# Kernel optimization log

Hardware: AMD Instinct MI355X
Metric: run time of the kernel (lower is better)

## Reference

```python
import jax, jax.numpy as jnp
import numpy as np

DIM = 1024
NUM_HEADS = 16
DPH = DIM // NUM_HEADS
B, S = 4, 2048
LN_EPS = 1e-5


def layer_norm(x, g, b):
    mu = jnp.mean(x, axis=-1, keepdims=True)
    var = jnp.mean((x - mu) ** 2, axis=-1, keepdims=True)
    return (x - mu) * jax.lax.rsqrt(var + LN_EPS) * g + b


def setup_inputs() -> dict:
    key = jax.random.key(0)
    ks = jax.random.split(key, 10)
    sd = 0.02
    return {
        "x": jax.random.normal(ks[0], (B, S, DIM), dtype=jnp.float32),
        "Wq": jax.random.normal(ks[1], (DIM, DIM), dtype=jnp.float32) * sd,
        "Wk": jax.random.normal(ks[2], (DIM, DIM), dtype=jnp.float32) * sd,
        "Wv": jax.random.normal(ks[3], (DIM, DIM), dtype=jnp.float32) * sd,
        "bq": jnp.zeros((DIM,), dtype=jnp.float32),
        "bk": jnp.zeros((DIM,), dtype=jnp.float32),
        "bv": jnp.zeros((DIM,), dtype=jnp.float32),
        "ln1_g": jnp.ones((DIM,), dtype=jnp.float32),
        "ln1_b": jnp.zeros((DIM,), dtype=jnp.float32),
        "W1": jax.random.normal(ks[4], (DIM, 4 * DIM), dtype=jnp.float32) * sd,
        "b1": jnp.zeros((4 * DIM,), dtype=jnp.float32),
        "W2": jax.random.normal(ks[5], (4 * DIM, DIM), dtype=jnp.float32) * sd,
        "b2": jnp.zeros((DIM,), dtype=jnp.float32),
        "ln2_g": jnp.ones((DIM,), dtype=jnp.float32),
        "ln2_b": jnp.zeros((DIM,), dtype=jnp.float32),
    }


def reference(x, Wq, Wk, Wv, bq, bk, bv, ln1_g, ln1_b, W1, b1, W2, b2, ln2_g, ln2_b):
    b, s, d = x.shape
    # QKV projections (heads are independent linears -> one fused GEMM each)
    q = (x @ Wq + bq).reshape(b, s, NUM_HEADS, DPH)
    k = (x @ Wk + bk).reshape(b, s, NUM_HEADS, DPH)
    v = (x @ Wv + bv).reshape(b, s, NUM_HEADS, DPH)
    # Faithful quirk: module scales by 1/sqrt(dph) twice => 1/dph total
    scores = jnp.einsum("bqhd,bkhd->bhqk", q, k) / DPH
    causal = jnp.tril(jnp.ones((s, s), dtype=bool))
    scores = jnp.where(causal, scores, -1e9)
    attn = jax.nn.softmax(scores, axis=-1)
    out_attn = jnp.einsum("bhqk,bkhd->bqhd", attn, v).reshape(b, s, d)
    # Add & Norm 1 (no output projection in original)
    h = layer_norm(out_attn + x, ln1_g, ln1_b)
    # Feed-forward (dropout is identity at eval)
    ffn = jax.nn.relu(h @ W1 + b1) @ W2 + b2
    # Add & Norm 2
    return layer_norm(ffn + h, ln2_g, ln2_b)
```

## Files before the change

### kernel.cpp

```cpp
#include <hip/hip_runtime.h>
#include <hip/hip_bf16.h>

typedef __bf16 bf16_t;
typedef __bf16 bf16x8 __attribute__((ext_vector_type(8)));
typedef __bf16 bf16x4 __attribute__((ext_vector_type(4)));
typedef float  floatx4 __attribute__((ext_vector_type(4)));

#define DIM    1024
#define S_LEN  2048
#define NHEAD  16

template <typename T>
__device__ __forceinline__ bf16x8 load8bf(const T* src) {
  if constexpr (sizeof(T) == 2) {
    return *reinterpret_cast<const bf16x8*>(src);
  } else {
    floatx4 f0 = *reinterpret_cast<const floatx4*>(src);
    floatx4 f1 = *reinterpret_cast<const floatx4*>(src + 4);
    bf16x8 h;
    h[0] = (bf16_t)f0[0]; h[1] = (bf16_t)f0[1];
    h[2] = (bf16_t)f0[2]; h[3] = (bf16_t)f0[3];
    h[4] = (bf16_t)f1[0]; h[5] = (bf16_t)f1[1];
    h[6] = (bf16_t)f1[2]; h[7] = (bf16_t)f1[3];
    return h;
  }
}

__device__ __forceinline__ void gll16(const bf16_t* g, bf16_t* l) {
  __builtin_amdgcn_global_load_lds(
      (const __attribute__((address_space(1))) void*)g,
      (__attribute__((address_space(3))) void*)l, 16, 0, 0);
}

__global__ __launch_bounds__(256) void conv_bf(const float* __restrict__ in,
                                               bf16_t* __restrict__ out) {
  size_t i = ((size_t)blockIdx.x * 256 + threadIdx.x) * 8;
  *reinterpret_cast<bf16x8*>(out + i) = load8bf(in + i);
}

__global__ __launch_bounds__(256) void convT3(
    const float* __restrict__ in0, int ldi0, bf16_t* __restrict__ out0,
    const float* __restrict__ in1, int ldi1, bf16_t* __restrict__ out1,
    const float* __restrict__ in2, int ldi2, bf16_t* __restrict__ out2,
    int ldo) {
  __shared__ bf16_t tile[32][33];
  const int z = blockIdx.z;
  const float* in = (z == 0) ? in0 : ((z == 1) ? in1 : in2);
  bf16_t* out = (z == 0) ? out0 : ((z == 1) ? out1 : out2);
  int ldi = (z == 0) ? ldi0 : ((z == 1) ? ldi1 : ldi2);
  int tx = threadIdx.x, ty = threadIdx.y;
  int n0 = blockIdx.x * 32, k0 = blockIdx.y * 32;
#pragma unroll
  for (int i = 0; i < 4; ++i)
    tile[ty + 8 * i][tx] = (bf16_t)in[(size_t)(k0 + ty + 8 * i) * ldi + n0 + tx];
  __syncthreads();
#pragma unroll
  for (int i = 0; i < 4; ++i)
    out[(size_t)(n0 + ty + 8 * i) * ldo + k0 + tx] = tile[tx][ty + 8 * i];
}

#define BM 128
#define BN 128
#define BK 32
#define LSTR 40

template <typename TA>
__global__ __launch_bounds__(256) void gemm_abt(
    const TA* __restrict__ A, int lda,
    const bf16_t* __restrict__ Bt, int zBRow,
    bf16_t* __restrict__ C, int ldc, int zCOff,
    const float* __restrict__ bias0, const float* __restrict__ bias1,
    const float* __restrict__ bias2,
    int K, int relu, int accum) {
  constexpr int ASTR = (sizeof(TA) == 2) ? BK : LSTR;
  __shared__ bf16_t As[BM * LSTR];
  __shared__ bf16_t Bs[BN * BK];
  const int z = blockIdx.z;
  const float* bias = (z == 0) ? bias0 : ((z == 1) ? bias1 : bias2);
  const bf16_t* Bz = Bt + (size_t)z * zBRow * K;
  C += (size_t)z * zCOff;

  const int tid  = threadIdx.x;
  const int lane = tid & 63;
  const int wave = tid >> 6;
  const int wr   = wave >> 1;
  const int wc   = wave & 1;
  const int quad = lane >> 4;
  const int l15  = lane & 15;
  const int m0   = blockIdx.y * BM;
  const int n0   = blockIdx.x * BN;

  floatx4 acc[4][4];
#pragma unroll
  for (int i = 0; i < 4; ++i)
#pragma unroll
    for (int j = 0; j < 4; ++j) acc[i][j] = (floatx4)(0.0f);

  const int kIters = K / BK;
  for (int kt = 0; kt < kIters; ++kt) {
#pragma unroll
    for (int i = 0; i < 2; ++i)
      gll16(Bz + (size_t)(n0 + wave * 32 + i * 16 + (lane >> 2)) * K +
                kt * BK + (lane & 3) * 8,
            &Bs[(wave * 32 + i * 16) * BK]);
    if constexpr (sizeof(TA) == 2) {
#pragma unroll
      for (int i = 0; i < 2; ++i)
        gll16(A + (size_t)(m0 + wave * 32 + i * 16 + (lane >> 2)) * lda +
                  kt * BK + (lane & 3) * 8,
              &As[(wave * 32 + i * 16) * BK]);
    } else {
#pragma unroll
      for (int p = 0; p < 2; ++p) {
        int id  = p * 256 + tid;
        int row = id >> 2;
        int c8  = (id & 3) * 8;
        *reinterpret_cast<bf16x8*>(&As[row * LSTR + c8]) =
            load8bf(A + (size_t)(m0 + row) * lda + kt * BK + c8);
      }
    }
    __syncthreads();

    bf16x8 a[4], b[4];
#pragma unroll
    for (int i = 0; i < 4; ++i)
      a[i] = *reinterpret_cast<const bf16x8*>(
          &As[(wr * 64 + i * 16 + l15) * ASTR + quad * 8]);
#pragma unroll
    for (int j = 0; j < 4; ++j)
      b[j] = *reinterpret_cast<const bf16x8*>(
          &Bs[(wc * 64 + j * 16 + l15) * BK + quad * 8]);
#pragma unroll
    for (int i = 0; i < 4; ++i)
#pragma unroll
      for (int j = 0; j < 4; ++j)
        acc[i][j] = __builtin_amdgcn_mfma_f32_16x16x32_bf16(a[i], b[j], acc[i][j], 0, 0, 0);
    __syncthreads();
  }

#pragma unroll
  for (int j = 0; j < 4; ++j) {
    int gn = n0 + wc * 64 + j * 16 + l15;
    float bv = bias ? bias[gn] : 0.0f;
#pragma unroll
    for (int i = 0; i < 4; ++i) {
      int gm = m0 + wr * 64 + i * 16 + quad * 4;
#pragma unroll
      for (int r = 0; r < 4; ++r) {
        float v = acc[i][j][r] + bv;
        if (relu) v = fmaxf(v, 0.0f);
        size_t idx = (size_t)(gm + r) * ldc + gn;
        if (accum) v += (float)C[idx];
        C[idx] = (bf16_t)v;
      }
    }
  }
}

__global__ __launch_bounds__(256) void transpose_v(const bf16_t* __restrict__ in,
                                                   bf16_t* __restrict__ outp) {
  __shared__ bf16_t tile[32][33];
  int tx = threadIdx.x, ty = threadIdx.y;
  int s0 = blockIdx.x * 32, d0 = blockIdx.y * 32, bh = blockIdx.z;
  int z = bh >> 4, h = bh & 15;
  const bf16_t* src = in + (size_t)z * S_LEN * 3072 + 2048 + h * 64;
#pragma unroll
  for (int i = 0; i < 4; ++i)
    tile[ty + 8 * i][tx] = src[(size_t)(s0 + ty + 8 * i) * 3072 + d0 + tx];
  __syncthreads();
  bf16_t* dst = outp + (size_t)bh * 64 * S_LEN;
#pragma unroll
  for (int i = 0; i < 4; ++i)
    dst[(size_t)(d0 + ty + 8 * i) * S_LEN + s0 + tx] = tile[tx][ty + 8 * i];
}

#define TQ  64
#define TK  64
#define AST 72
#define QSCALE 0.02254211f

struct KVregs { bf16x8 k[2]; bf16x8 v[2]; };

__global__ __launch_bounds__(256, 2) void attn_mfma2(
    const bf16_t* __restrict__ qkv, const bf16_t* __restrict__ vt,
    float* __restrict__ out) {
  __shared__ bf16_t QsPs[TQ * AST];
  __shared__ bf16_t Ks[TK * AST];
  __shared__ bf16_t Vs[TK * AST];

  const int tid  = threadIdx.x;
  const int lane = tid & 63;
  const int w    = tid >> 6;
  const int quad = lane >> 4;
  const int l15  = lane & 15;
  const int pi   = blockIdx.x;
  const int h    = blockIdx.y;
  const int z    = blockIdx.z;
  const int qb2[2] = {pi, 31 - pi};
  const bf16_t* qkv_b = qkv + (size_t)z * S_LEN * 3072;
  const bf16_t* vt_bh = vt + ((size_t)z * NHEAD + h) * 64 * S_LEN;
  float* out_b = out + (size_t)z * S_LEN * DIM;

  const int ktEnd = qb2[1] + 1;

  auto kv_load = [&](KVregs& r, int kt) {
#pragma unroll
    for (int p = 0; p < 2; ++p) {
      int id  = p * 256 + tid;
      int row = id >> 3;
      int c8  = (id & 7) * 8;
      r.k[p] = *reinterpret_cast<const bf16x8*>(
          qkv_b + (size_t)(kt * TK + row) * 3072 + 1024 + h * 64 + c8);
      r.v[p] = *reinterpret_cast<const bf16x8*>(
          vt_bh + (size_t)row * S_LEN + kt * TK + c8);
    }
  };
  auto kv_write = [&](KVregs& r) {
#pragma unroll
    for (int p = 0; p < 2; ++p) {
      int id  = p * 256 + tid;
      int row = id >> 3;
      int c8  = (id & 7) * 8;
      *reinterpret_cast<bf16x8*>(&Ks[row * AST + c8]) = r.k[p];
      *reinterpret_cast<bf16x8*>(&Vs[row * AST + c8]) = r.v[p];
    }
  };

  KVregs RA, RB;
  kv_load(RA, 0);

  bf16x8 aq[2][2];
  for (int tile = 0; tile < 2; ++tile) {
    if (tile) __syncthreads();
    const int qg0 = qb2[tile] * TQ;
#pragma unroll
    for (int p = 0; p < 2; ++p) {
      int id  = p * 256 + tid;
      int row = id >> 3;
      int c8  = (id & 7) * 8;
      bf16x8 v = *reinterpret_cast<const bf16x8*>(
          qkv_b + (size_t)(qg0 + row) * 3072 + h * 64 + c8);
      bf16x8 o;
#pragma unroll
      for (int e = 0; e < 8; ++e) o[e] = (bf16_t)((float)v[e] * QSCALE);
      *reinterpret_cast<bf16x8*>(&QsPs[row * AST + c8]) = o;
    }
    __syncthreads();
#pragma unroll
    for (int ks = 0; ks < 2; ++ks)
      aq[tile][ks] = *reinterpret_cast<const bf16x8*>(
          &QsPs[(w * 16 + l15) * AST + ks * 32 + quad * 8]);
  }

  float lp[2][4];
  floatx4 O[2][4];
#pragma unroll
  for (int t = 0; t < 2; ++t)
#pragma unroll
    for (int r = 0; r < 4; ++r) lp[t][r] = 0.0f;
#pragma unroll
  for (int t = 0; t < 2; ++t)
#pragma unroll
    for (int dt = 0; dt < 4; ++dt) O[t][dt] = (floatx4)(0.0f);

  auto step = [&](int kt, KVregs& cur, KVregs& nxt) {
    if (kt + 1 < ktEnd) kv_load(nxt, kt + 1);
    asm volatile("s_waitcnt lgkmcnt(0)" ::: "memory");
    __builtin_amdgcn_s_barrier();
    kv_write(cur);
    asm volatile("s_waitcnt lgkmcnt(0)" ::: "memory");
    __builtin_amdgcn_s_barrier();

    bf16x8 bk[4][2], bv[4][2];
#pragma unroll
    for (int i = 0; i < 4; ++i)
#pragma unroll
      for (int ks = 0; ks < 2; ++ks) {
        bk[i][ks] = *reinterpret_cast<const bf16x8*>(
            &Ks[(i * 16 + l15) * AST + ks * 32 + quad * 8]);
        bv[i][ks] = *reinterpret_cast<const bf16x8*>(
            &Vs[(i * 16 + l15) * AST + ks * 32 + quad * 8]);
      }

#pragma unroll
    for (int tile = 0; tile < 2; ++tile) {
      const int qtb = qb2[tile] * TQ + w * 16;
      if (kt * TK > qtb + 15) continue;

      floatx4 s[4];
      __builtin_amdgcn_s_setprio(1);
#pragma unroll
      for (int ktl = 0; ktl < 4; ++ktl) {
        s[ktl] = __builtin_amdgcn_mfma_f32_16x16x32_bf16(
            aq[tile][0], bk[ktl][0], (floatx4)(0.0f), 0, 0, 0);
        s[ktl] = __builtin_amdgcn_mfma_f32_16x16x32_bf16(
            aq[tile][1], bk[ktl][1], s[ktl], 0, 0, 0);
      }
      __builtin_amdgcn_s_setprio(0);
      if (kt * TK + TK - 1 > qtb) {
#pragma unroll
        for (int ktl = 0; ktl < 4; ++ktl) {
          int gk = kt * TK + ktl * 16 + l15;
#pragma unroll
          for (int r = 0; r < 4; ++r) {
            int gq = qtb + quad * 4 + r;
            if (gk > gq) s[ktl][r] = -1e30f;
          }
        }
      }
#pragma unroll
      for (int ktl = 0; ktl < 4; ++ktl)
#pragma unroll
        for (int r = 0; r < 4; ++r) {
          float p = exp2f(s[ktl][r]);
          lp[tile][r] += p;
          QsPs[(w * 16 + quad * 4 + r) * AST + ktl * 16 + l15] = (bf16_t)p;
        }

      bf16x8 ap0 = *reinterpret_cast<const bf16x8*>(
          &QsPs[(w * 16 + l15) * AST + quad * 8]);
      bf16x8 ap1 = *reinterpret_cast<const bf16x8*>(
          &QsPs[(w * 16 + l15) * AST + 32 + quad * 8]);
      __builtin_amdgcn_s_setprio(1);
#pragma unroll
      for (int dt = 0; dt < 4; ++dt) {
        O[tile][dt] = __builtin_amdgcn_mfma_f32_16x16x32_bf16(
            ap0, bv[dt][0], O[tile][dt], 0, 0, 0);
        O[tile][dt] = __builtin_amdgcn_mfma_f32_16x16x32_bf16(
            ap1, bv[dt][1], O[tile][dt], 0, 0, 0);
      }
      __builtin_amdgcn_s_setprio(0);
    }
  };

  for (int kt = 0; kt < ktEnd; kt += 2) {
    step(kt, RA, RB);
    if (kt + 1 < ktEnd) step(kt + 1, RB, RA);
  }

#pragma unroll
  for (int tile = 0; tile < 2; ++tile) {
    const int qg0 = qb2[tile] * TQ;
    float inv[4];
#pragma unroll
    for (int r = 0; r < 4; ++r) {
      float lv = lp[tile][r];
#pragma unroll
      for (int off = 1; off < 16; off <<= 1) lv += __shfl_xor(lv, off);
      inv[r] = 1.0f / lv;
    }
#pragma unroll
    for (int dt = 0; dt < 4; ++dt)
#pragma unroll
      for (int r = 0; r < 4; ++r)
        out_b[(size_t)(qg0 + w * 16 + quad * 4 + r) * DIM +
              h * 64 + dt * 16 + l15] = O[tile][dt][r] * inv[r];
  }
}

template <typename TA>
__global__ __launch_bounds__(256) void add_ln_k(const TA* a,
                                                const float* b,
                                                const float* __restrict__ g,
                                                const float* __restrict__ be,
                                                float* out) {
  const int row = blockIdx.x;
  const int t   = threadIdx.x;
  const size_t base = (size_t)row * DIM;

  float x[4];
  {
    floatx4 bv = *reinterpret_cast<const floatx4*>(b + base + t * 4);
    if constexpr (sizeof(TA) == 2) {
      bf16x4 av = *reinterpret_cast<const bf16x4*>(a + base + t * 4);
#pragma unroll
      for (int i = 0; i < 4; ++i) x[i] = (float)av[i] + bv[i];
    } else {
      floatx4 av = *reinterpret_cast<const floatx4*>(a + base + t * 4);
#pragma unroll
      for (int i = 0; i < 4; ++i) x[i] = av[i] + bv[i];
    }
  }
  float s1 = 0.0f, s2 = 0.0f;
#pragma unroll
  for (int i = 0; i < 4; ++i) { s1 += x[i]; s2 += x[i] * x[i]; }
#pragma unroll
  for (int off = 32; off; off >>= 1) {
    s1 += __shfl_xor(s1, off);
    s2 += __shfl_xor(s2, off);
  }
  __shared__ float ls1[4], ls2[4];
  if ((t & 63) == 0) { ls1[t >> 6] = s1; ls2[t >> 6] = s2; }
  __syncthreads();
  float S1 = ls1[0] + ls1[1] + ls1[2] + ls1[3];
  float S2 = ls2[0] + ls2[1] + ls2[2] + ls2[3];
  float mu  = S1 * (1.0f / DIM);
  float var = S2 * (1.0f / DIM) - mu * mu;
  float rs  = rsqrtf(var + 1e-5f);
#pragma unroll
  for (int i = 0; i < 4; ++i) {
    int c = t * 4 + i;
    out[base + c] = (x[i] - mu) * rs * g[c] + be[c];
  }
}

extern "C" void kernel_launch(void* const* d_in, const int* in_sizes, int n_in,
                              void* d_out, int out_size, void* d_ws, size_t ws_size,
                              hipStream_t stream) {
  const float* x   = (const float*)d_in[0];
  const float* Wq  = (const float*)d_in[1];
  const float* Wk  = (const float*)d_in[2];
  const float* Wv  = (const float*)d_in[3];
  const float* bq  = (const float*)d_in[4];
  const float* bk  = (const float*)d_in[5];
  const float* bv  = (const float*)d_in[6];
  const float* g1  = (const float*)d_in[7];
  const float* be1 = (const float*)d_in[8];
  const float* W1  = (const float*)d_in[9];
  const float* b1  = (const float*)d_in[10];
  const float* W2  = (const float*)d_in[11];
  const float* b2  = (const float*)d_in[12];
  const float* g2  = (const float*)d_in[13];
  const float* be2 = (const float*)d_in[14];
  float* out = (float*)d_out;
  char*  ws  = (char*)d_ws;

  bf16_t* WqkvT = (bf16_t*)(ws);
  bf16_t* qkv2  = (bf16_t*)(ws + 6291456);
  bf16_t* vt    = (bf16_t*)(ws + 31457280);
  bf16_t* xbf   = (bf16_t*)(ws + 31457280);
  bf16_t* W1Tq  = (bf16_t*)(ws);
  bf16_t* W2Tq  = (bf16_t*)(ws + 2097152);
  bf16_t* mid   = (bf16_t*)(ws + 4194304);
  bf16_t* ffnO  = (bf16_t*)(ws + 20971520);

  dim3 tb(32, 8);
  convT3<<<dim3(32, 32, 3), tb, 0, stream>>>(
      Wq, 1024, WqkvT, Wk, 1024, WqkvT + 1048576, Wv, 1024, WqkvT + 2097152, 1024);

  for (int p = 0; p < 2; ++p) {
    const float* xp   = x   + (size_t)p * 2 * S_LEN * DIM;
    float*       outp = out + (size_t)p * 2 * S_LEN * DIM;
    conv_bf<<<2048, 256, 0, stream>>>(xp, xbf);
    gemm_abt<bf16_t><<<dim3(8, 32, 3), 256, 0, stream>>>(
        xbf, 1024, WqkvT, 1024, qkv2, 3072, 1024, bq, bk, bv, 1024, 0, 0);
    transpose_v<<<dim3(64, 2, 32), tb, 0, stream>>>(qkv2, vt);
    attn_mfma2<<<dim3(16, 16, 2), 256, 0, stream>>>(qkv2, vt, outp);
  }
  add_ln_k<float><<<8192, 256, 0, stream>>>(out, x, g1, be1, out);

  for (int q = 0; q < 4; ++q) {
    convT3<<<dim3(32, 32, 2), tb, 0, stream>>>(
        W1 + q * 1024, 4096, W1Tq,
        W2 + (size_t)q * 1024 * 1024, 1024, W2Tq,
        nullptr, 0, nullptr, 1024);
    gemm_abt<float><<<dim3(8, 64, 1), 256, 0, stream>>>(
        out, 1024, W1Tq, 0, mid, 1024, 0, b1 + q * 1024, nullptr, nullptr,
        1024, 1, 0);
    gemm_abt<bf16_t><<<dim3(8, 64, 1), 256, 0, stream>>>(
        mid, 1024, W2Tq, 0, ffnO, 1024, 0, (q == 0) ? b2 : nullptr, nullptr,
        nullptr, 1024, 0, (q > 0) ? 1 : 0);
  }
  add_ln_k<bf16_t><<<8192, 256, 0, stream>>>(ffnO, out, g2, be2, out);
}
```

Measured before the change: 718.3 us.

## Double-buffer GEMM LDS tiles and XOR-swizzle B/A columns to avoid bank conflicts

Converts the GEMM main loop to a two-stage LDS double buffer: the next K tile is issued (direct global-to-LDS for bf16, register prefetch for fp32 A) before the MFMAs on the current tile, cutting one barrier per iteration and overlapping loads with compute. It also XOR-swizzles the 16-byte chunk column on writes and reads of bf16 tiles to reduce LDS bank conflicts. This doubles LDS use, which may lower occupancy, and adds register pressure for the fp32 prefetch path.

```diff
diff --git a/kernel.cpp b/kernel.cpp
--- a/kernel.cpp
+++ b/kernel.cpp
@@ -72,9 +72,10 @@
     const float* __restrict__ bias0, const float* __restrict__ bias1,
     const float* __restrict__ bias2,
     int K, int relu, int accum) {
-  constexpr int ASTR = (sizeof(TA) == 2) ? BK : LSTR;
-  __shared__ bf16_t As[BM * LSTR];
-  __shared__ bf16_t Bs[BN * BK];
+  constexpr bool FAST = (sizeof(TA) == 2);
+  constexpr int ASTR = FAST ? BK : LSTR;
+  __shared__ bf16_t As[2][BM * LSTR];
+  __shared__ bf16_t Bs[2][BN * BK];
   const int z = blockIdx.z;
   const float* bias = (z == 0) ? bias0 : ((z == 1) ? bias1 : bias2);
   const bf16_t* Bz = Bt + (size_t)z * zBRow * K;
@@ -89,53 +90,103 @@
   const int l15  = lane & 15;
   const int m0   = blockIdx.y * BM;
   const int n0   = blockIdx.x * BN;
-
-  floatx4 acc[4][4];
-#pragma unroll
-  for (int i = 0; i < 4; ++i)
-#pragma unroll
-    for (int j = 0; j < 4; ++j) acc[i][j] = (floatx4)(0.0f);
-
-  const int kIters = K / BK;
-  for (int kt = 0; kt < kIters; ++kt) {
+  const int swz = ((lane & 3) ^ ((lane >> 3) & 3)) * 8;
+  const int rsw = (l15 >> 1) & 3;
+
+  auto stageB = [&](int buf, int kt) {
 #pragma unroll
     for (int i = 0; i < 2; ++i)
       gll16(Bz + (size_t)(n0 + wave * 32 + i * 16 + (lane >> 2)) * K +
-                kt * BK + (lane & 3) * 8,
-            &Bs[(wave * 32 + i * 16) * BK]);
-    if constexpr (sizeof(TA) == 2) {
-#pragma unroll
-      for (int i = 0; i < 2; ++i)
-        gll16(A + (size_t)(m0 + wave * 32 + i * 16 + (lane >> 2)) * lda +
-                  kt * BK + (lane & 3) * 8,
-              &As[(wave * 32 + i * 16) * BK]);
-    } else {
-#pragma unroll
-      for (int p = 0; p < 2; ++p) {
-        int id  = p * 256 + tid;
-        int row = id >> 2;
-        int c8  = (id & 3) * 8;
-        *reinterpret_cast<bf16x8*>(&As[row * LSTR + c8]) =
-            load8bf(A + (size_t)(m0 + row) * lda + kt * BK + c8);
-      }
-    }
-    __syncthreads();
+                kt * BK + swz,
+            &Bs[buf][(wave * 32 + i * 16) * BK]);
+  };
+  auto stageAfast = [&](int buf, int kt) {
+#pragma unroll
+    for (int i = 0; i < 2; ++i)
+      gll16(reinterpret_cast<const bf16_t*>(A) +
+                (size_t)(m0 + wave * 32 + i * 16 + (lane >> 2)) * lda +
+                kt * BK + swz,
+            &As[buf][(wave * 32 + i * 16) * BK]);
+  };
+  floatx4 fa0[2], fa1[2];
+  auto loadAreg = [&](int kt) {
+#pragma unroll
+    for (int p = 0; p < 2; ++p) {
+      int id  = p * 256 + tid;
+      int row = id >> 2;
+      int c8  = (id & 3) * 8;
+      const float* src = reinterpret_cast<const float*>(A) +
+                         (size_t)(m0 + row) * lda + kt * BK + c8;
+      fa0[p] = *reinterpret_cast<const floatx4*>(src);
+      fa1[p] = *reinterpret_cast<const floatx4*>(src + 4);
+    }
+  };
+  auto writeAreg = [&](int buf) {
+#pragma unroll
+    for (int p = 0; p < 2; ++p) {
+      int id  = p * 256 + tid;
+      int row = id >> 2;
+      int c8  = (id & 3) * 8;
+      bf16x8 h;
+      h[0] = (bf16_t)fa0[p][0]; h[1] = (bf16_t)fa0[p][1];
+      h[2] = (bf16_t)fa0[p][2]; h[3] = (bf16_t)fa0[p][3];
+      h[4] = (bf16_t)fa1[p][0]; h[5] = (bf16_t)fa1[p][1];
+      h[6] = (bf16_t)fa1[p][2]; h[7] = (bf16_t)fa1[p][3];
+      *reinterpret_cast<bf16x8*>(&As[buf][row * LSTR + c8]) = h;
+    }
+  };
+
+  floatx4 acc[4][4];
+#pragma unroll
+  for (int i = 0; i < 4; ++i)
+#pragma unroll
+    for (int j = 0; j < 4; ++j) acc[i][j] = (floatx4)(0.0f);
+
+  const int kIters = K / BK;
+  stageB(0, 0);
+  if constexpr (FAST) {
+    stageAfast(0, 0);
+  } else {
+    loadAreg(0);
+    writeAreg(0);
+  }
+  __syncthreads();
+
+  int cur = 0;
+  for (int kt = 0; kt < kIters; ++kt) {
+    const int nxt = cur ^ 1;
+    const bool pre = (kt + 1 < kIters);
+    if (pre) {
+      stageB(nxt, kt + 1);
+      if constexpr (FAST) stageAfast(nxt, kt + 1);
+      else loadAreg(kt + 1);
+    }
 
     bf16x8 a[4], b[4];
 #pragma unroll
-    for (int i = 0; i < 4; ++i)
-      a[i] = *reinterpret_cast<const bf16x8*>(
-          &As[(wr * 64 + i * 16 + l15) * ASTR + quad * 8]);
+    for (int i = 0; i < 4; ++i) {
+      if constexpr (FAST)
+        a[i] = *reinterpret_cast<const bf16x8*>(
+            &As[cur][(wr * 64 + i * 16 + l15) * BK + (quad ^ rsw) * 8]);
+      else
+        a[i] = *reinterpret_cast<const bf16x8*>(
+            &As[cur][(wr * 64 + i * 16 + l15) * LSTR + quad * 8]);
+    }
 #pragma unroll
     for (int j = 0; j < 4; ++j)
       b[j] = *reinterpret_cast<const bf16x8*>(
-          &Bs[(wc * 64 + j * 16 + l15) * BK + quad * 8]);
+          &Bs[cur][(wc * 64 + j * 16 + l15) * BK + (quad ^ rsw) * 8]);
 #pragma unroll
     for (int i = 0; i < 4; ++i)
 #pragma unroll
       for (int j = 0; j < 4; ++j)
         acc[i][j] = __builtin_amdgcn_mfma_f32_16x16x32_bf16(a[i], b[j], acc[i][j], 0, 0, 0);
+
+    if constexpr (!FAST) {
+      if (pre) writeAreg(nxt);
+    }
     __syncthreads();
+    cur = nxt;
   }
 
 #pragma unroll
```

Measured after the change: 692.4 us. -3.6%, faster.

## Double-buffer GEMM LDS with swizzle, XCD remap, bf16 LN output for FFN

Applied to the files above, without the earlier changes.

GEMM now double-buffers LDS tiles with async global-to-LDS loads and an XOR swizzle to cut bank conflicts, and drops the fp32-A conversion path. Blocks of GEMM and attention kernels are remapped across XCDs for cache locality. The first LayerNorm also emits a bf16 copy of h used directly by the FFN GEMM, and FFN output accumulates in fp32 into the output buffer, removing the separate ffn buffer. Risks swizzle mismatch and extra fp32 read-modify-write traffic.

```diff
diff --git a/kernel.cpp b/kernel.cpp
--- a/kernel.cpp
+++ b/kernel.cpp
@@ -32,6 +32,18 @@
       (__attribute__((address_space(3))) void*)l, 16, 0, 0);
 }
 
+__device__ __forceinline__ void xcd_remap(int& bx, int& by, int& bz) {
+  const int gx = gridDim.x, gy = gridDim.y, gz = gridDim.z;
+  const int nwg = gx * gy * gz;
+  int lin = ((int)blockIdx.z * gy + blockIdx.y) * gx + blockIdx.x;
+  int cid = lin;
+  if ((nwg & 7) == 0) cid = (lin & 7) * (nwg >> 3) + (lin >> 3);
+  bx = cid % gx;
+  int t = cid / gx;
+  bz = t % gz;
+  by = t / gz;
+}
+
 __global__ __launch_bounds__(256) void conv_bf(const float* __restrict__ in,
                                                bf16_t* __restrict__ out) {
   size_t i = ((size_t)blockIdx.x * 256 + threadIdx.x) * 8;
@@ -62,20 +74,21 @@
 #define BM 128
 #define BN 128
 #define BK 32
-#define LSTR 40
-
-template <typename TA>
+
+template <typename TC>
 __global__ __launch_bounds__(256) void gemm_abt(
-    const TA* __restrict__ A, int lda,
+    const bf16_t* __restrict__ A, int lda,
     const bf16_t* __restrict__ Bt, int zBRow,
-    bf16_t* __restrict__ C, int ldc, int zCOff,
+    TC* __restrict__ C, int ldc, int zCOff,
     const float* __restrict__ bias0, const float* __restrict__ bias1,
     const float* __restrict__ bias2,
     int K, int relu, int accum) {
-  constexpr int ASTR = (sizeof(TA) == 2) ? BK : LSTR;
-  __shared__ bf16_t As[BM * LSTR];
-  __shared__ bf16_t Bs[BN * BK];
-  const int z = blockIdx.z;
+  __shared__ bf16_t As[2][BM * BK];
+  __shared__ bf16_t Bs[2][BN * BK];
+
+  int bx, by, bz;
+  xcd_remap(bx, by, bz);
+  const int z = bz;
   const float* bias = (z == 0) ? bias0 : ((z == 1) ? bias1 : bias2);
   const bf16_t* Bz = Bt + (size_t)z * zBRow * K;
   C += (size_t)z * zCOff;
@@ -87,55 +100,62 @@
   const int wc   = wave & 1;
   const int quad = lane >> 4;
   const int l15  = lane & 15;
-  const int m0   = blockIdx.y * BM;
-  const int n0   = blockIdx.x * BN;
-
-  floatx4 acc[4][4];
-#pragma unroll
-  for (int i = 0; i < 4; ++i)
-#pragma unroll
-    for (int j = 0; j < 4; ++j) acc[i][j] = (floatx4)(0.0f);
-
-  const int kIters = K / BK;
-  for (int kt = 0; kt < kIters; ++kt) {
+  const int m0   = by * BM;
+  const int n0   = bx * BN;
+  const int swz = ((lane & 3) ^ ((lane >> 3) & 3)) * 8;
+  const int rsw = (l15 >> 1) & 3;
+
+  auto stageB = [&](int buf, int kt) {
 #pragma unroll
     for (int i = 0; i < 2; ++i)
       gll16(Bz + (size_t)(n0 + wave * 32 + i * 16 + (lane >> 2)) * K +
-                kt * BK + (lane & 3) * 8,
-            &Bs[(wave * 32 + i * 16) * BK]);
-    if constexpr (sizeof(TA) == 2) {
-#pragma unroll
-      for (int i = 0; i < 2; ++i)
-        gll16(A + (size_t)(m0 + wave * 32 + i * 16 + (lane >> 2)) * lda +
-                  kt * BK + (lane & 3) * 8,
-              &As[(wave * 32 + i * 16) * BK]);
-    } else {
-#pragma unroll
-      for (int p = 0; p < 2; ++p) {
-        int id  = p * 256 + tid;
-        int row = id >> 2;
-        int c8  = (id & 3) * 8;
-        *reinterpret_cast<bf16x8*>(&As[row * LSTR + c8]) =
-            load8bf(A + (size_t)(m0 + row) * lda + kt * BK + c8);
-      }
-    }
-    __syncthreads();
+                kt * BK + swz,
+            &Bs[buf][(wave * 32 + i * 16) * BK]);
+  };
+  auto stageA = [&](int buf, int kt) {
+#pragma unroll
+    for (int i = 0; i < 2; ++i)
+      gll16(A + (size_t)(m0 + wave * 32 + i * 16 + (lane >> 2)) * lda +
+                kt * BK + swz,
+            &As[buf][(wave * 32 + i * 16) * BK]);
+  };
+
+  floatx4 acc[4][4];
+#pragma unroll
+  for (int i = 0; i < 4; ++i)
+#pragma unroll
+    for (int j = 0; j < 4; ++j) acc[i][j] = (floatx4)(0.0f);
+
+  const int kIters = K / BK;
+  stageB(0, 0);
+  stageA(0, 0);
+  __syncthreads();
+
+  int cur = 0;
+  for (int kt = 0; kt < kIters; ++kt) {
+    const int nxt = cur ^ 1;
+    if (kt + 1 < kIters) {
+      stageB(nxt, kt + 1);
+      stageA(nxt, kt + 1);
+    }
 
     bf16x8 a[4], b[4];
 #pragma unroll
     for (int i = 0; i < 4; ++i)
       a[i] = *reinterpret_cast<const bf16x8*>(
-          &As[(wr * 64 + i * 16 + l15) * ASTR + quad * 8]);
+          &As[cur][(wr * 64 + i * 16 + l15) * BK + (quad ^ rsw) * 8]);
 #pragma unroll
     for (int j = 0; j < 4; ++j)
       b[j] = *reinterpret_cast<const bf16x8*>(
-          &Bs[(wc * 64 + j * 16 + l15) * BK + quad * 8]);
+          &Bs[cur][(wc * 64 + j * 16 + l15) * BK + (quad ^ rsw) * 8]);
 #pragma unroll
     for (int i = 0; i < 4; ++i)
 #pragma unroll
       for (int j = 0; j < 4; ++j)
         acc[i][j] = __builtin_amdgcn_mfma_f32_16x16x32_bf16(a[i], b[j], acc[i][j], 0, 0, 0);
+
     __syncthreads();
+    cur = nxt;
   }
 
 #pragma unroll
@@ -151,7 +171,7 @@
         if (relu) v = fmaxf(v, 0.0f);
         size_t idx = (size_t)(gm + r) * ldc + gn;
         if (accum) v += (float)C[idx];
-        C[idx] = (bf16_t)v;
+        C[idx] = (TC)v;
       }
     }
   }
@@ -193,9 +213,8 @@
   const int w    = tid >> 6;
   const int quad = lane >> 4;
   const int l15  = lane & 15;
-  const int pi   = blockIdx.x;
-  const int h    = blockIdx.y;
-  const int z    = blockIdx.z;
+  int pi, h, z;
+  xcd_remap(pi, h, z);
   const int qb2[2] = {pi, 31 - pi};
   const bf16_t* qkv_b = qkv + (size_t)z * S_LEN * 3072;
   const bf16_t* vt_bh = vt + ((size_t)z * NHEAD + h) * 64 * S_LEN;
@@ -363,7 +382,8 @@
                                                 const float* b,
                                                 const float* __restrict__ g,
                                                 const float* __restrict__ be,
-                                                float* out) {
+                                                float* out,
+                                                bf16_t* __restrict__ bfout) {
   const int row = blockIdx.x;
   const int t   = threadIdx.x;
   const size_t base = (size_t)row * DIM;
@@ -371,14 +391,19 @@
   float x[4];
   {
     floatx4 bv = *reinterpret_cast<const floatx4*>(b + base + t * 4);
-    if constexpr (sizeof(TA) == 2) {
-      bf16x4 av = *reinterpret_cast<const bf16x4*>(a + base + t * 4);
-#pragma unroll
-      for (int i = 0; i < 4; ++i) x[i] = (float)av[i] + bv[i];
+    if (a) {
+      if constexpr (sizeof(TA) == 2) {
+        bf16x4 av = *reinterpret_cast<const bf16x4*>(a + base + t * 4);
+#pragma unroll
+        for (int i = 0; i < 4; ++i) x[i] = (float)av[i] + bv[i];
+      } else {
+        floatx4 av = *reinterpret_cast<const floatx4*>(a + base + t * 4);
+#pragma unroll
+        for (int i = 0; i < 4; ++i) x[i] = av[i] + bv[i];
+      }
     } else {
-      floatx4 av = *reinterpret_cast<const floatx4*>(a + base + t * 4);
-#pragma unroll
-      for (int i = 0; i < 4; ++i) x[i] = av[i] + bv[i];
+#pragma unroll
+      for (int i = 0; i < 4; ++i) x[i] = bv[i];
     }
   }
   float s1 = 0.0f, s2 = 0.0f;
@@ -400,7 +425,9 @@
 #pragma unroll
   for (int i = 0; i < 4; ++i) {
     int c = t * 4 + i;
-    out[base + c] = (x[i] - mu) * rs * g[c] + be[c];
+    float hv = (x[i] - mu) * rs * g[c] + be[c];
+    out[base + c] = hv;
+    if (bfout) bfout[base + c] = (bf16_t)hv;
   }
 }
 
@@ -431,8 +458,8 @@
   bf16_t* xbf   = (bf16_t*)(ws + 31457280);
   bf16_t* W1Tq  = (bf16_t*)(ws);
   bf16_t* W2Tq  = (bf16_t*)(ws + 2097152);
-  bf16_t* mid   = (bf16_t*)(ws + 4194304);
-  bf16_t* ffnO  = (bf16_t*)(ws + 20971520);
+  bf16_t* hbf   = (bf16_t*)(ws + 4194304);
+  bf16_t* mid   = (bf16_t*)(ws + 20971520);
 
   dim3 tb(32, 8);
   convT3<<<dim3(32, 32, 3), tb, 0, stream>>>(
@@ -447,19 +474,19 @@
     transpose_v<<<dim3(64, 2, 32), tb, 0, stream>>>(qkv2, vt);
     attn_mfma2<<<dim3(16, 16, 2), 256, 0, stream>>>(qkv2, vt, outp);
   }
-  add_ln_k<float><<<8192, 256, 0, stream>>>(out, x, g1, be1, out);
+  add_ln_k<float><<<8192, 256, 0, stream>>>(out, x, g1, be1, out, hbf);
 
   for (int q = 0; q < 4; ++q) {
     convT3<<<dim3(32, 32, 2), tb, 0, stream>>>(
         W1 + q * 1024, 4096, W1Tq,
         W2 + (size_t)q * 1024 * 1024, 1024, W2Tq,
         nullptr, 0, nullptr, 1024);
+    gemm_abt<bf16_t><<<dim3(8, 64, 1), 256, 0, stream>>>(
+        hbf, 1024, W1Tq, 0, mid, 1024, 0, b1 + q * 1024, nullptr, nullptr,
+        1024, 1, 0);
     gemm_abt<float><<<dim3(8, 64, 1), 256, 0, stream>>>(
-        out, 1024, W1Tq, 0, mid, 1024, 0, b1 + q * 1024, nullptr, nullptr,
-        1024, 1, 0);
-    gemm_abt<bf16_t><<<dim3(8, 64, 1), 256, 0, stream>>>(
-        mid, 1024, W2Tq, 0, ffnO, 1024, 0, (q == 0) ? b2 : nullptr, nullptr,
-        nullptr, 1024, 0, (q > 0) ? 1 : 0);
-  }
-  add_ln_k<bf16_t><<<8192, 256, 0, stream>>>(ffnO, out, g2, be2, out);
-}
+        mid, 1024, W2Tq, 0, out, 1024, 0, (q == 0) ? b2 : nullptr, nullptr,
+        nullptr, 1024, 0, 1);
+  }
+  add_ln_k<float><<<8192, 256, 0, stream>>>(nullptr, out, g2, be2, out, nullptr);
+}
```

After: 666.6 us. -7.2%, faster.
